# Kernel tuning notes

Measured on AMD Instinct MI355X. Metric: run time of the kernel, lower is better.

Reference implementation:

```python
import jax, jax.numpy as jnp
import numpy as np

N, E, F_IN, D, H = 20000, 640000, 128, 16, 8  # nodes, edges, in_features, out_features, n_heads


def _linear_params(k, fan_in, fan_out):
    W = jax.random.normal(k, (fan_in, fan_out), jnp.float32) / np.sqrt(fan_in)
    b = jnp.zeros((fan_out,), jnp.float32)
    return W, b


def setup_inputs() -> dict:
    key = jax.random.key(0)
    ks = jax.random.split(key, 8)
    x = jax.random.normal(ks[0], (N, F_IN), jnp.float32)
    edge_index = jax.random.randint(ks[1], (2, E), 0, N, dtype=jnp.int64)
    Wq, bq = _linear_params(ks[2], F_IN, D * H)
    Wk, bk = _linear_params(ks[3], F_IN, D * H)
    Wv, bv = _linear_params(ks[4], F_IN, D * H)
    Wpsi, bpsi = _linear_params(ks[5], D, D)
    Wo, bo = _linear_params(ks[6], D * H * 2, F_IN)
    gamma = jnp.ones((F_IN,), jnp.float32)
    beta = jnp.zeros((F_IN,), jnp.float32)
    return {"x": x, "edge_index": edge_index, "Wq": Wq, "bq": bq, "Wk": Wk, "bk": bk,
            "Wv": Wv, "bv": bv, "Wpsi": Wpsi, "bpsi": bpsi, "Wo": Wo, "bo": bo,
            "gamma": gamma, "beta": beta}


def _segment_softmax(logits, seg, num_segments):
    # numerically-stable softmax of edge logits grouped by destination node (row)
    m = jax.ops.segment_max(logits, seg, num_segments=num_segments)  # [N,H]
    m = jnp.where(jnp.isfinite(m), m, 0.0)
    e = jnp.exp(logits - m[seg])  # [E,H]
    s = jax.ops.segment_sum(e, seg, num_segments=num_segments)  # [N,H]
    return e / (s[seg] + 1e-16)


def reference(x, edge_index, Wq, bq, Wk, bk, Wv, bv, Wpsi, bpsi, Wo, bo, gamma, beta):
    q = (x @ Wq + bq).reshape(N, H, D)
    k = (x @ Wk + bk).reshape(N, H, D)
    v = (x @ Wv + bv).reshape(N, H, D)
    row, col = edge_index[0], edge_index[1]

    logits = jnp.einsum('ehd,ehd->eh', q[row], k[col]) / np.sqrt(D)  # [E,H]
    alpha = _segment_softmax(logits, row, N)  # [E,H]

    v_j = v[col]  # [E,H,D]
    h_lp = jax.ops.segment_sum((alpha[..., None] * v_j).reshape(E, H * D), row, num_segments=N)
    v_bp = jnp.tanh(v_j @ Wpsi + bpsi)  # per-head linear on last dim, [E,H,D]
    h_bp = jax.ops.segment_sum((alpha[..., None] * v_bp).reshape(E, H * D), row, num_segments=N)

    h_out = jnp.concatenate([h_lp, h_bp], axis=1) @ Wo + bo  # [N,F_IN]
    y = x + jax.nn.relu(h_out)
    mu = jnp.mean(y, axis=-1, keepdims=True)
    var = jnp.mean(jnp.square(y - mu), axis=-1, keepdims=True)
    return (y - mu) * jax.lax.rsqrt(var + 1e-5) * gamma + beta
```

## Files before the change

### kernel.cpp

```cpp
#include <hip/hip_runtime.h>
#include <hip/hip_bf16.h>
#include <math.h>

#define NN 20000
#define EE 640000

typedef __attribute__((ext_vector_type(8))) short short8;
typedef __attribute__((ext_vector_type(4))) float f32x4;
typedef __hip_bfloat16 bf16;
typedef __hip_bfloat162 bf162;

__device__ inline ushort f2bf(float f) {
  bf16 h = __float2bfloat16(f);
  return *(ushort*)&h;
}
__device__ inline float2 ldbf2(const ushort* p) {
  return __bfloat1622float2(*(const bf162*)p);
}
__device__ inline float2 bf2u(uint u) {
  return __bfloat1622float2(*(const bf162*)&u);
}


__global__ __launch_bounds__(256) void qkv_mfma(
    const float* __restrict__ x,
    const float* __restrict__ Wq, const float* __restrict__ bq,
    const float* __restrict__ Wk, const float* __restrict__ bk,
    const float* __restrict__ Wv, const float* __restrict__ bv,
    float* __restrict__ qbuf, ushort* __restrict__ kvb) {
  __shared__ ushort As[128 * 136];
  __shared__ ushort Bts[128 * 136];
  int t = threadIdx.x;
  int n0 = blockIdx.x * 128;
  int mat = blockIdx.y;
  const float* W    = mat == 0 ? Wq : (mat == 1 ? Wk : Wv);
  const float* bias = mat == 0 ? bq : (mat == 1 ? bk : bv);

  {
    int r = t >> 1, half = (t & 1) * 64;
    int n = n0 + r;
    ushort* dst = &As[r * 136 + half];
    if (n < NN) {
      const float* src = x + (size_t)n * 128 + half;
#pragma unroll
      for (int j = 0; j < 8; ++j) {
        float4 f0 = *(const float4*)(src + 8 * j);
        float4 f1 = *(const float4*)(src + 8 * j + 4);
        ushort tmp[8] = {f2bf(f0.x), f2bf(f0.y), f2bf(f0.z), f2bf(f0.w),
                         f2bf(f1.x), f2bf(f1.y), f2bf(f1.z), f2bf(f1.w)};
        *(uint4*)(dst + 8 * j) = *(uint4*)tmp;
      }
    } else {
#pragma unroll
      for (int j = 0; j < 8; ++j) *(uint4*)(dst + 8 * j) = make_uint4(0, 0, 0, 0);
    }
  }
  {
    int k = t >> 1, nh = (t & 1) * 64;
    const float* src = W + (size_t)k * 128 + nh;
#pragma unroll
    for (int i = 0; i < 16; ++i) {
      float4 f = *(const float4*)(src + 4 * i);
      Bts[(nh + 4 * i + 0) * 136 + k] = f2bf(f.x);
      Bts[(nh + 4 * i + 1) * 136 + k] = f2bf(f.y);
      Bts[(nh + 4 * i + 2) * 136 + k] = f2bf(f.z);
      Bts[(nh + 4 * i + 3) * 136 + k] = f2bf(f.w);
    }
  }
  __syncthreads();

  int w = t >> 6, lane = t & 63;
  int m = lane & 15, q = lane >> 4;
  int r0 = w * 32;
  f32x4 acc0[8], acc1[8];
#pragma unroll
  for (int c = 0; c < 8; ++c) {
    acc0[c] = (f32x4){0.f, 0.f, 0.f, 0.f};
    acc1[c] = (f32x4){0.f, 0.f, 0.f, 0.f};
  }
#pragma unroll
  for (int kb = 0; kb < 4; ++kb) {
    int kof = kb * 32 + 8 * q;
    short8 a0 = *(const short8*)&As[(r0 + m) * 136 + kof];
    short8 a1 = *(const short8*)&As[(r0 + 16 + m) * 136 + kof];
#pragma unroll
    for (int c = 0; c < 8; ++c) {
      short8 b = *(const short8*)&Bts[(c * 16 + m) * 136 + kof];
      acc0[c] = __builtin_amdgcn_mfma_f32_16x16x32_bf16(a0, b, acc0[c], 0, 0, 0);
      acc1[c] = __builtin_amdgcn_mfma_f32_16x16x32_bf16(a1, b, acc1[c], 0, 0, 0);
    }
  }
  int koff2 = (mat == 2) ? 2 : 0;
#pragma unroll
  for (int c = 0; c < 8; ++c) {
    int col = c * 16 + m;
    float bb = bias[col];
    size_t pos = (size_t)(col >> 1) * 6 + (col & 1) + koff2;
#pragma unroll
    for (int reg = 0; reg < 4; ++reg) {
      int row0 = n0 + r0 + 4 * q + reg;
      int row1 = row0 + 16;
      float v0 = acc0[c][reg] + bb;
      float v1 = acc1[c][reg] + bb;
      if (mat == 0) {
        if (row0 < NN) qbuf[(size_t)row0 * 128 + col] = v0;
        if (row1 < NN) qbuf[(size_t)row1 * 128 + col] = v1;
      } else {
        if (row0 < NN) kvb[(size_t)row0 * 384 + pos] = f2bf(v0);
        if (row1 < NN) kvb[(size_t)row1 * 384 + pos] = f2bf(v1);
      }
    }
  }
}

__global__ __launch_bounds__(256) void vb_kernel(
    ushort* __restrict__ kvb,
    const float* __restrict__ Wpsi, const float* __restrict__ bpsi) {
  __shared__ float Ws[256];
  __shared__ float bs[16];
  int t = threadIdx.x;
  Ws[t] = Wpsi[t];
  if (t < 16) bs[t] = bpsi[t];
  __syncthreads();
  int idx = blockIdx.x * 256 + t;
  int n = idx >> 3, h = idx & 7;
  ushort* base = kvb + (size_t)n * 384 + (size_t)h * 48;
  float v[16];
#pragma unroll
  for (int dp = 0; dp < 8; ++dp) {
    float2 f = ldbf2(base + dp * 6 + 2);
    v[2 * dp] = f.x; v[2 * dp + 1] = f.y;
  }
  float o[16];
#pragma unroll
  for (int d = 0; d < 16; ++d) o[d] = bs[d];
#pragma unroll
  for (int dp = 0; dp < 16; ++dp) {
    float vv = v[dp];
#pragma unroll
    for (int d = 0; d < 16; ++d) o[d] = fmaf(vv, Ws[dp * 16 + d], o[d]);
  }
#pragma unroll
  for (int dp = 0; dp < 8; ++dp) {
    uint u = (uint)f2bf(tanhf(o[2 * dp])) | ((uint)f2bf(tanhf(o[2 * dp + 1])) << 16);
    *(uint*)(base + dp * 6 + 4) = u;
  }
}

__global__ __launch_bounds__(256) void scatter_pad(const int* __restrict__ ei,
                                                   int* __restrict__ cursor,
                                                   int* __restrict__ scol) {
  int e = blockIdx.x * 256 + threadIdx.x;
  if (e < EE) {
    int r = ei[e];
    int c = ei[EE + e];
    int pos = atomicAdd(&cursor[r], 1);
    if (pos < 128) scol[r * 128 + pos] = c;
  }
}

__global__ __launch_bounds__(256) void aggregate_kernel(
    const float* __restrict__ qbuf, const ushort* __restrict__ kvb,
    const int* __restrict__ cursor, const int* __restrict__ scol,
    float* __restrict__ hbuf) {
  int wid = threadIdx.x >> 6, lane = threadIdx.x & 63;
  int node = blockIdx.x * 4 + wid;
  int h = lane >> 3, dg = (lane & 7) * 2;
  int off = h * 16 + dg;
  const float SC = 0.25f * 1.44269504f;
  float2 q2 = *(const float2*)(qbuf + (size_t)node * 128 + off);
  q2.x *= SC; q2.y *= SC;
  int cnt = cursor[node];
  cnt = cnt > 128 ? 128 : cnt;
  int base = node * 128;
  const char* kvbase = (const char*)kvb + lane * 12;
  float s = 0.f, aV0 = 0.f, aV1 = 0.f, aB0 = 0.f, aB1 = 0.f;

  struct U3 { uint x, y, z; };
  auto ldu = [&](int j) -> U3 {
    return *(const U3*)(kvbase + (size_t)j * 768);
  };
  auto proc = [&](U3 u) {
    float2 kk = bf2u(u.x);
    float2 vv = bf2u(u.y);
    float2 tb = bf2u(u.z);
    float d = fmaf(q2.x, kk.x, q2.y * kk.y);
    d += __shfl_xor(d, 1);
    d += __shfl_xor(d, 2);
    d += __shfl_xor(d, 4);
    float wgt = exp2f(d);
    s += wgt;
    aV0 = fmaf(wgt, vv.x, aV0); aV1 = fmaf(wgt, vv.y, aV1);
    aB0 = fmaf(wgt, tb.x, aB0); aB1 = fmaf(wgt, tb.y, aB1);
  };

  int i = 0;
  for (; i + 8 <= cnt; i += 8) {
    int4 ja = *(const int4*)&scol[base + i];
    int4 jb = *(const int4*)&scol[base + i + 4];
    U3 u0 = ldu(ja.x), u1 = ldu(ja.y), u2 = ldu(ja.z), u3 = ldu(ja.w);
    U3 u4 = ldu(jb.x), u5 = ldu(jb.y), u6 = ldu(jb.z), u7 = ldu(jb.w);
    proc(u0); proc(u1); proc(u2); proc(u3);
    proc(u4); proc(u5); proc(u6); proc(u7);
  }
  if (i + 4 <= cnt) {
    int4 ja = *(const int4*)&scol[base + i];
    U3 u0 = ldu(ja.x), u1 = ldu(ja.y), u2 = ldu(ja.z), u3 = ldu(ja.w);
    proc(u0); proc(u1); proc(u2); proc(u3);
    i += 4;
  }
  for (; i < cnt; ++i) proc(ldu(scol[base + i]));

  float inv = s > 0.f ? 1.f / s : 0.f;
  float* hp = hbuf + (size_t)node * 256 + off;
  *(float2*)(hp)       = make_float2(aV0 * inv, aV1 * inv);
  *(float2*)(hp + 128) = make_float2(aB0 * inv, aB1 * inv);
}

__global__ __launch_bounds__(256) void output_mfma(
    const float* __restrict__ hbuf, const float* __restrict__ x,
    const float* __restrict__ Wo, const float* __restrict__ bo,
    const float* __restrict__ gamma, const float* __restrict__ beta,
    float* __restrict__ out) {
  __shared__ ushort As[128 * 136];
  __shared__ ushort Bts[128 * 136];
  __shared__ float bos[128], gs[128], bts[128];
  int t = threadIdx.x;
  int n0 = blockIdx.x * 128;
  if (t < 128) { bos[t] = bo[t]; gs[t] = gamma[t]; bts[t] = beta[t]; }
  int w = t >> 6, lane = t & 63;
  int m = lane & 15, q = lane >> 4;
  int r0 = w * 32;
  f32x4 acc0[8], acc1[8];
#pragma unroll
  for (int c = 0; c < 8; ++c) {
    acc0[c] = (f32x4){0.f, 0.f, 0.f, 0.f};
    acc1[c] = (f32x4){0.f, 0.f, 0.f, 0.f};
  }
  for (int kc = 0; kc < 2; ++kc) {
    if (kc) __syncthreads();
    {
      int r = t >> 1, half = (t & 1) * 64;
      int n = n0 + r;
      ushort* dst = &As[r * 136 + half];
      if (n < NN) {
        const float* src = hbuf + (size_t)n * 256 + kc * 128 + half;
#pragma unroll
        for (int j = 0; j < 8; ++j) {
          float4 f0 = *(const float4*)(src + 8 * j);
          float4 f1 = *(const float4*)(src + 8 * j + 4);
          ushort tmp[8] = {f2bf(f0.x), f2bf(f0.y), f2bf(f0.z), f2bf(f0.w),
                           f2bf(f1.x), f2bf(f1.y), f2bf(f1.z), f2bf(f1.w)};
          *(uint4*)(dst + 8 * j) = *(uint4*)tmp;
        }
      } else {
#pragma unroll
        for (int j = 0; j < 8; ++j) *(uint4*)(dst + 8 * j) = make_uint4(0, 0, 0, 0);
      }
    }
    {
      int k = t >> 1, nh = (t & 1) * 64;
      const float* src = Wo + (size_t)(kc * 128 + k) * 128 + nh;
#pragma unroll
      for (int i = 0; i < 16; ++i) {
        float4 f = *(const float4*)(src + 4 * i);
        Bts[(nh + 4 * i + 0) * 136 + k] = f2bf(f.x);
        Bts[(nh + 4 * i + 1) * 136 + k] = f2bf(f.y);
        Bts[(nh + 4 * i + 2) * 136 + k] = f2bf(f.z);
        Bts[(nh + 4 * i + 3) * 136 + k] = f2bf(f.w);
      }
    }
    __syncthreads();
#pragma unroll
    for (int kb = 0; kb < 4; ++kb) {
      int kof = kb * 32 + 8 * q;
      short8 a0 = *(const short8*)&As[(r0 + m) * 136 + kof];
      short8 a1 = *(const short8*)&As[(r0 + 16 + m) * 136 + kof];
#pragma unroll
      for (int c = 0; c < 8; ++c) {
        short8 b = *(const short8*)&Bts[(c * 16 + m) * 136 + kof];
        acc0[c] = __builtin_amdgcn_mfma_f32_16x16x32_bf16(a0, b, acc0[c], 0, 0, 0);
        acc1[c] = __builtin_amdgcn_mfma_f32_16x16x32_bf16(a1, b, acc1[c], 0, 0, 0);
      }
    }
  }
#pragma unroll
  for (int half = 0; half < 2; ++half) {
#pragma unroll
    for (int reg = 0; reg < 4; ++reg) {
      int row = n0 + r0 + half * 16 + 4 * q + reg;
      bool valid = row < NN;
      float vals[8];
      float sum = 0.f;
#pragma unroll
      for (int c = 0; c < 8; ++c) {
        int col = c * 16 + m;
        float a = (half ? acc1[c][reg] : acc0[c][reg]) + bos[col];
        a = fmaxf(a, 0.f);
        float xv = valid ? x[(size_t)row * 128 + col] : 0.f;
        float v = a + xv;
        vals[c] = v;
        sum += v;
      }
      sum += __shfl_xor(sum, 1); sum += __shfl_xor(sum, 2);
      sum += __shfl_xor(sum, 4); sum += __shfl_xor(sum, 8);
      float mean = sum * (1.f / 128.f);
      float ssq = 0.f;
#pragma unroll
      for (int c = 0; c < 8; ++c) {
        float d = vals[c] - mean;
        ssq = fmaf(d, d, ssq);
      }
      ssq += __shfl_xor(ssq, 1); ssq += __shfl_xor(ssq, 2);
      ssq += __shfl_xor(ssq, 4); ssq += __shfl_xor(ssq, 8);
      float rstd = rsqrtf(ssq * (1.f / 128.f) + 1e-5f);
      if (valid) {
#pragma unroll
        for (int c = 0; c < 8; ++c) {
          int col = c * 16 + m;
          out[(size_t)row * 128 + col] = (vals[c] - mean) * rstd * gs[col] + bts[col];
        }
      }
    }
  }
}

extern "C" void kernel_launch(void* const* d_in, const int* in_sizes, int n_in,
                              void* d_out, int out_size, void* d_ws, size_t ws_size,
                              hipStream_t stream) {
  const float* x     = (const float*)d_in[0];
  const int*   ei    = (const int*)d_in[1];
  const float* Wq    = (const float*)d_in[2];
  const float* bq    = (const float*)d_in[3];
  const float* Wk    = (const float*)d_in[4];
  const float* bk    = (const float*)d_in[5];
  const float* Wv    = (const float*)d_in[6];
  const float* bv    = (const float*)d_in[7];
  const float* Wpsi  = (const float*)d_in[8];
  const float* bpsi  = (const float*)d_in[9];
  const float* Wo    = (const float*)d_in[10];
  const float* bo    = (const float*)d_in[11];
  const float* gamma = (const float*)d_in[12];
  const float* beta  = (const float*)d_in[13];
  float* out = (float*)d_out;

  char* ws = (char*)d_ws;
  float*  qbuf   = (float*) (ws);
  ushort* kvb    = (ushort*)(ws + 10240000);
  float*  hbuf   = (float*) (ws + 25600000);
  int*    cursor = (int*)   (ws + 46080000);
  int*    scol   = (int*)   (ws + 46160000);

  hipMemsetAsync(cursor, 0, 80000, stream);

  qkv_mfma<<<dim3(157, 3), 256, 0, stream>>>(x, Wq, bq, Wk, bk, Wv, bv, qbuf, kvb);
  vb_kernel<<<625, 256, 0, stream>>>(kvb, Wpsi, bpsi);
  scatter_pad<<<2500, 256, 0, stream>>>(ei, cursor, scol);
  aggregate_kernel<<<5000, 256, 0, stream>>>(qbuf, kvb, cursor, scol, hbuf);
  output_mfma<<<157, 256, 0, stream>>>(hbuf, x, Wo, bo, gamma, beta, out);
}
```

Measured before the change: 235.4 us.

## Bucket neighbor lists by source chunk and shrink aggregation buffers to 16-bit

Edges are now bucketed per destination node into 16 column chunks, with up to 16 slots each and 16-bit column indices. The aggregation kernel gives each wave four nodes and walks the chunks in order, with a block barrier after each chunk, to make the gathered K/V rows more cache-local. The scatter is fused into the V-basis kernel's launch, and the cursor memset moves into the QKV kernel. The aggregated features are written as bf16, so the output GEMM loads them directly without converting. In exchange, per-chunk loops are very short, which adds loop overhead and divergence, and neighbors beyond 16 per chunk are silently dropped.

```diff
diff --git a/kernel.cpp b/kernel.cpp
--- a/kernel.cpp
+++ b/kernel.cpp
@@ -4,6 +4,9 @@
 
 #define NN 20000
 #define EE 640000
+#define NCH 16
+#define CHN 1250
+#define SLOT 16
 
 typedef __attribute__((ext_vector_type(8))) short short8;
 typedef __attribute__((ext_vector_type(4))) float f32x4;
@@ -27,10 +30,15 @@
     const float* __restrict__ Wq, const float* __restrict__ bq,
     const float* __restrict__ Wk, const float* __restrict__ bk,
     const float* __restrict__ Wv, const float* __restrict__ bv,
-    float* __restrict__ qbuf, ushort* __restrict__ kvb) {
+    float* __restrict__ qbuf, ushort* __restrict__ kvb,
+    int* __restrict__ cursor2) {
   __shared__ ushort As[128 * 136];
   __shared__ ushort Bts[128 * 136];
   int t = threadIdx.x;
+  {
+    int flat = (blockIdx.y * 157 + blockIdx.x) * 256 + t;
+    for (int j = flat; j < NN * NCH; j += 157 * 3 * 256) cursor2[j] = 0;
+  }
   int n0 = blockIdx.x * 128;
   int mat = blockIdx.y;
   const float* W    = mat == 0 ? Wq : (mat == 1 ? Wk : Wv);
@@ -113,16 +121,30 @@
   }
 }
 
-__global__ __launch_bounds__(256) void vb_kernel(
+__global__ __launch_bounds__(256) void vb_scatter(
     ushort* __restrict__ kvb,
-    const float* __restrict__ Wpsi, const float* __restrict__ bpsi) {
+    const float* __restrict__ Wpsi, const float* __restrict__ bpsi,
+    const int* __restrict__ ei,
+    int* __restrict__ cursor2, ushort* __restrict__ scol2) {
   __shared__ float Ws[256];
   __shared__ float bs[16];
   int t = threadIdx.x;
+  int bid = blockIdx.x;
+  if (bid < 2500) {
+    int e = bid * 256 + t;
+    if (e < EE) {
+      int r = ei[e];
+      int c = ei[EE + e];
+      int ch = c / CHN;
+      int pos = atomicAdd(&cursor2[r * NCH + ch], 1);
+      if (pos < SLOT) scol2[((size_t)r * NCH + ch) * SLOT + pos] = (ushort)c;
+    }
+    return;
+  }
   Ws[t] = Wpsi[t];
   if (t < 16) bs[t] = bpsi[t];
   __syncthreads();
-  int idx = blockIdx.x * 256 + t;
+  int idx = (bid - 2500) * 256 + t;
   int n = idx >> 3, h = idx & 7;
   ushort* base = kvb + (size_t)n * 384 + (size_t)h * 48;
   float v[16];
@@ -147,78 +169,78 @@
   }
 }
 
-__global__ __launch_bounds__(256) void scatter_pad(const int* __restrict__ ei,
-                                                   int* __restrict__ cursor,
-                                                   int* __restrict__ scol) {
-  int e = blockIdx.x * 256 + threadIdx.x;
-  if (e < EE) {
-    int r = ei[e];
-    int c = ei[EE + e];
-    int pos = atomicAdd(&cursor[r], 1);
-    if (pos < 128) scol[r * 128 + pos] = c;
-  }
-}
-
 __global__ __launch_bounds__(256) void aggregate_kernel(
     const float* __restrict__ qbuf, const ushort* __restrict__ kvb,
-    const int* __restrict__ cursor, const int* __restrict__ scol,
-    float* __restrict__ hbuf) {
+    const int* __restrict__ cursor2, const ushort* __restrict__ scol2,
+    ushort* __restrict__ hbufb) {
   int wid = threadIdx.x >> 6, lane = threadIdx.x & 63;
-  int node = blockIdx.x * 4 + wid;
+  int wg = blockIdx.x * 4 + wid;
+  int n0 = wg * 4;
   int h = lane >> 3, dg = (lane & 7) * 2;
   int off = h * 16 + dg;
   const float SC = 0.25f * 1.44269504f;
-  float2 q2 = *(const float2*)(qbuf + (size_t)node * 128 + off);
-  q2.x *= SC; q2.y *= SC;
-  int cnt = cursor[node];
-  cnt = cnt > 128 ? 128 : cnt;
-  int base = node * 128;
+
+  float q2x[4], q2y[4], s[4], aV0[4], aV1[4], aB0[4], aB1[4];
+#pragma unroll
+  for (int ni = 0; ni < 4; ++ni) {
+    float2 q2 = *(const float2*)(qbuf + (size_t)(n0 + ni) * 128 + off);
+    q2x[ni] = q2.x * SC; q2y[ni] = q2.y * SC;
+    s[ni] = 0.f; aV0[ni] = 0.f; aV1[ni] = 0.f; aB0[ni] = 0.f; aB1[ni] = 0.f;
+  }
+  int mycnt = cursor2[n0 * NCH + lane];
+  mycnt = mycnt > SLOT ? SLOT : mycnt;
+
   const char* kvbase = (const char*)kvb + lane * 12;
-  float s = 0.f, aV0 = 0.f, aV1 = 0.f, aB0 = 0.f, aB1 = 0.f;
-
   struct U3 { uint x, y, z; };
-  auto ldu = [&](int j) -> U3 {
-    return *(const U3*)(kvbase + (size_t)j * 768);
-  };
-  auto proc = [&](U3 u) {
-    float2 kk = bf2u(u.x);
-    float2 vv = bf2u(u.y);
-    float2 tb = bf2u(u.z);
-    float d = fmaf(q2.x, kk.x, q2.y * kk.y);
-    d += __shfl_xor(d, 1);
-    d += __shfl_xor(d, 2);
-    d += __shfl_xor(d, 4);
-    float wgt = exp2f(d);
-    s += wgt;
-    aV0 = fmaf(wgt, vv.x, aV0); aV1 = fmaf(wgt, vv.y, aV1);
-    aB0 = fmaf(wgt, tb.x, aB0); aB1 = fmaf(wgt, tb.y, aB1);
-  };
-
-  int i = 0;
-  for (; i + 8 <= cnt; i += 8) {
-    int4 ja = *(const int4*)&scol[base + i];
-    int4 jb = *(const int4*)&scol[base + i + 4];
-    U3 u0 = ldu(ja.x), u1 = ldu(ja.y), u2 = ldu(ja.z), u3 = ldu(ja.w);
-    U3 u4 = ldu(jb.x), u5 = ldu(jb.y), u6 = ldu(jb.z), u7 = ldu(jb.w);
-    proc(u0); proc(u1); proc(u2); proc(u3);
-    proc(u4); proc(u5); proc(u6); proc(u7);
-  }
-  if (i + 4 <= cnt) {
-    int4 ja = *(const int4*)&scol[base + i];
-    U3 u0 = ldu(ja.x), u1 = ldu(ja.y), u2 = ldu(ja.z), u3 = ldu(ja.w);
-    proc(u0); proc(u1); proc(u2); proc(u3);
-    i += 4;
-  }
-  for (; i < cnt; ++i) proc(ldu(scol[base + i]));
-
-  float inv = s > 0.f ? 1.f / s : 0.f;
-  float* hp = hbuf + (size_t)node * 256 + off;
-  *(float2*)(hp)       = make_float2(aV0 * inv, aV1 * inv);
-  *(float2*)(hp + 128) = make_float2(aB0 * inv, aB1 * inv);
+
+  for (int ch = 0; ch < NCH; ++ch) {
+#pragma unroll
+    for (int ni = 0; ni < 4; ++ni) {
+      int cnt = __shfl(mycnt, ni * 16 + ch);
+      if (cnt == 0) continue;
+      const ushort* sl = scol2 + ((size_t)(n0 + ni) * NCH + ch) * SLOT;
+      float lq2x = q2x[ni], lq2y = q2y[ni];
+      float ls = 0.f, lV0 = 0.f, lV1 = 0.f, lB0 = 0.f, lB1 = 0.f;
+      auto proc = [&](int e) {
+        U3 u = *(const U3*)(kvbase + (size_t)e * 768);
+        float2 kk = bf2u(u.x);
+        float2 vv = bf2u(u.y);
+        float2 tb = bf2u(u.z);
+        float d = fmaf(lq2x, kk.x, lq2y * kk.y);
+        d += __shfl_xor(d, 1);
+        d += __shfl_xor(d, 2);
+        d += __shfl_xor(d, 4);
+        float wgt = exp2f(d);
+        ls += wgt;
+        lV0 = fmaf(wgt, vv.x, lV0); lV1 = fmaf(wgt, vv.y, lV1);
+        lB0 = fmaf(wgt, tb.x, lB0); lB1 = fmaf(wgt, tb.y, lB1);
+      };
+      int i = 0;
+      for (; i + 2 <= cnt; i += 2) {
+        uint u = *(const uint*)(sl + i);
+        proc(u & 0xffff);
+        proc(u >> 16);
+      }
+      if (i < cnt) proc(sl[i]);
+      s[ni] += ls;
+      aV0[ni] += lV0; aV1[ni] += lV1; aB0[ni] += lB0; aB1[ni] += lB1;
+    }
+    __syncthreads();
+  }
+
+#pragma unroll
+  for (int ni = 0; ni < 4; ++ni) {
+    float inv = s[ni] > 0.f ? 1.f / s[ni] : 0.f;
+    ushort* hp = hbufb + (size_t)(n0 + ni) * 256 + off;
+    uint uv = (uint)f2bf(aV0[ni] * inv) | ((uint)f2bf(aV1[ni] * inv) << 16);
+    uint ub = (uint)f2bf(aB0[ni] * inv) | ((uint)f2bf(aB1[ni] * inv) << 16);
+    *(uint*)(hp)       = uv;
+    *(uint*)(hp + 128) = ub;
+  }
 }
 
 __global__ __launch_bounds__(256) void output_mfma(
-    const float* __restrict__ hbuf, const float* __restrict__ x,
+    const ushort* __restrict__ hbufb, const float* __restrict__ x,
     const float* __restrict__ Wo, const float* __restrict__ bo,
     const float* __restrict__ gamma, const float* __restrict__ beta,
     float* __restrict__ out) {
@@ -244,15 +266,10 @@
       int n = n0 + r;
       ushort* dst = &As[r * 136 + half];
       if (n < NN) {
-        const float* src = hbuf + (size_t)n * 256 + kc * 128 + half;
-#pragma unroll
-        for (int j = 0; j < 8; ++j) {
-          float4 f0 = *(const float4*)(src + 8 * j);
-          float4 f1 = *(const float4*)(src + 8 * j + 4);
-          ushort tmp[8] = {f2bf(f0.x), f2bf(f0.y), f2bf(f0.z), f2bf(f0.w),
-                           f2bf(f1.x), f2bf(f1.y), f2bf(f1.z), f2bf(f1.w)};
-          *(uint4*)(dst + 8 * j) = *(uint4*)tmp;
-        }
+        const ushort* src = hbufb + (size_t)n * 256 + kc * 128 + half;
+#pragma unroll
+        for (int j = 0; j < 8; ++j)
+          *(uint4*)(dst + 8 * j) = *(const uint4*)(src + 8 * j);
       } else {
 #pragma unroll
         for (int j = 0; j < 8; ++j) *(uint4*)(dst + 8 * j) = make_uint4(0, 0, 0, 0);
@@ -345,17 +362,15 @@
   float* out = (float*)d_out;
 
   char* ws = (char*)d_ws;
-  float*  qbuf   = (float*) (ws);
-  ushort* kvb    = (ushort*)(ws + 10240000);
-  float*  hbuf   = (float*) (ws + 25600000);
-  int*    cursor = (int*)   (ws + 46080000);
-  int*    scol   = (int*)   (ws + 46160000);
-
-  hipMemsetAsync(cursor, 0, 80000, stream);
-
-  qkv_mfma<<<dim3(157, 3), 256, 0, stream>>>(x, Wq, bq, Wk, bk, Wv, bv, qbuf, kvb);
-  vb_kernel<<<625, 256, 0, stream>>>(kvb, Wpsi, bpsi);
-  scatter_pad<<<2500, 256, 0, stream>>>(ei, cursor, scol);
-  aggregate_kernel<<<5000, 256, 0, stream>>>(qbuf, kvb, cursor, scol, hbuf);
-  output_mfma<<<157, 256, 0, stream>>>(hbuf, x, Wo, bo, gamma, beta, out);
-}
+  float*  qbuf    = (float*) (ws);
+  ushort* kvb     = (ushort*)(ws + 10240000);
+  ushort* hbufb   = (ushort*)(ws + 25600000);
+  int*    cursor2 = (int*)   (ws + 35840000);
+  ushort* scol2   = (ushort*)(ws + 37120000);
+
+  qkv_mfma<<<dim3(157, 3), 256, 0, stream>>>(x, Wq, bq, Wk, bk, Wv, bv,
+                                             qbuf, kvb, cursor2);
+  vb_scatter<<<3125, 256, 0, stream>>>(kvb, Wpsi, bpsi, ei, cursor2, scol2);
+  aggregate_kernel<<<1250, 256, 0, stream>>>(qbuf, kvb, cursor2, scol2, hbufb);
+  output_mfma<<<157, 256, 0, stream>>>(hbufb, x, Wo, bo, gamma, beta, out);
+}
```

Result: slower. 253.5 us (+7.7%).
